# Performance work log

Hardware: AMD Instinct MI355X
Metric: run time of the kernel (lower is better)

## Reference

```python
import jax, jax.numpy as jnp
import numpy as np

B, S, D, H, FF = 4, 1024, 1024, 16, 4096
HD = D // H
EPS = 1e-5


def _layernorm(x, g, b):
    m = x.mean(-1, keepdims=True)
    v = ((x - m) ** 2).mean(-1, keepdims=True)
    return g * (x - m) / jnp.sqrt(v + EPS) + b


def _heads(t):  # [B,S,D] -> [B,H,S,HD]
    return t.reshape(t.shape[0], t.shape[1], H, HD).transpose(0, 2, 1, 3)


def _attn(q, k, v):  # manual scaled-dot-product, returns [B,S,D]
    s = jnp.einsum('bhqd,bhkd->bhqk', q, k) / jnp.sqrt(jnp.float32(HD))
    a = jax.nn.softmax(s, axis=-1)
    o = jnp.einsum('bhqk,bhkd->bhqd', a, v)
    return o.transpose(0, 2, 1, 3).reshape(q.shape[0], q.shape[2], D)


def _proj(x, w, b):  # torch linear: x @ w.T + b
    return x @ w.T + b


def setup_inputs() -> dict:
    key = jax.random.key(0)
    ks = jax.random.split(key, 32)
    i = iter(range(32))
    act = lambda sh: jax.random.normal(ks[next(i)], sh, dtype=jnp.float32)
    wgt = lambda sh: jax.random.normal(ks[next(i)], sh, dtype=jnp.float32) * 0.02
    inp = {
        'x': act((B, S, D)), 'y': act((B, S, D)),
        'decoder_mask': jnp.zeros((1,), jnp.float32),
        'image_outputs': act((B, S, D)), 'constant_y': act((B, S, D)),
        'image_query_weight': wgt((D, D)), 'image_query_bias': wgt((D,)),
        'image_key_weight': wgt((D, D)), 'image_key_bias': wgt((D,)),
        'image_value_weight': wgt((D, D)), 'image_value_bias': wgt((D,)),
        'audio_query_weight': wgt((D, D)), 'audio_query_bias': wgt((D,)),
        'audio_key_weight': wgt((D, D)), 'audio_key_bias': wgt((D,)),
        'audio_value_weight': wgt((D, D)), 'audio_value_bias': wgt((D,)),
        'self_out_w': wgt((D, D)), 'self_out_b': wgt((D,)),
        'cross_out_w': wgt((D, D)), 'cross_out_b': wgt((D,)),
        'ffn_w1': wgt((FF, D)), 'ffn_b1': wgt((FF,)),
        'ffn_w2': wgt((D, FF)), 'ffn_b2': wgt((D,)),
        'gamma1': jnp.ones((D,), jnp.float32), 'beta1': jnp.zeros((D,), jnp.float32),
        'gamma2': jnp.ones((D,), jnp.float32), 'beta2': jnp.zeros((D,), jnp.float32),
        'gamma3': jnp.ones((D,), jnp.float32), 'beta3': jnp.zeros((D,), jnp.float32),
    }
    return inp


def reference(x, y, decoder_mask, image_outputs, constant_y,
              image_query_weight, image_query_bias, image_key_weight, image_key_bias,
              image_value_weight, image_value_bias,
              audio_query_weight, audio_query_bias, audio_key_weight, audio_key_bias,
              audio_value_weight, audio_value_bias,
              self_out_w, self_out_b, cross_out_w, cross_out_b,
              ffn_w1, ffn_b1, ffn_w2, ffn_b2,
              gamma1, beta1, gamma2, beta2, gamma3, beta3):
    # count == 0 path; mask is overwritten to None in the original; eval mode (no dropout)
    # --- self-attention: Q,K,V all from image_outputs with image weights ---
    q = _heads(_proj(image_outputs, image_query_weight, image_query_bias))
    k = _heads(_proj(image_outputs, image_key_weight, image_key_bias))
    v = _heads(_proj(image_outputs, image_value_weight, image_value_bias))
    sa = _proj(_attn(q, k, v), self_out_w, self_out_b)
    sa = jax.lax.stop_gradient(sa)  # out.detach().clone()
    y1 = _layernorm(sa + y, gamma1, beta1)
    # --- cross-attention: Q from constant_y (image query weights), K,V from x (audio weights) ---
    q = _heads(_proj(constant_y, image_query_weight, image_query_bias))
    k = _heads(_proj(x, audio_key_weight, audio_key_bias))
    v = _heads(_proj(x, audio_value_weight, audio_value_bias))
    ca = _proj(_attn(q, k, v), cross_out_w, cross_out_b)
    ca = jax.lax.stop_gradient(ca)
    y2 = _layernorm(ca + y1, gamma2, beta2)
    # --- FFN (hidden detached after relu in original) ---
    h = jax.lax.stop_gradient(jax.nn.relu(_proj(y2, ffn_w1, ffn_b1)))
    ff = _proj(h, ffn_w2, ffn_b2)
    y3 = _layernorm(ff + y2, gamma3, beta3)
    return y3
```

## Files before the change

kernel.cpp:

```cpp
#include <hip/hip_runtime.h>

typedef unsigned short u16;
typedef __attribute__((ext_vector_type(8))) short bf16x8;
typedef __attribute__((ext_vector_type(8))) unsigned short u16x8;
typedef __attribute__((ext_vector_type(4))) float f32x4;

__device__ __forceinline__ float bf2f(u16 x) {
  return __uint_as_float(((unsigned)x) << 16);
}
__device__ __forceinline__ u16 f2bf(float f) {
  unsigned u = __float_as_uint(f);
  unsigned r = (u + 0x7FFFu + ((u >> 16) & 1u)) >> 16;
  return (u16)r;
}

#define GLD_LDS16(g, l)                                                        \
  __builtin_amdgcn_global_load_lds(                                            \
      (const __attribute__((address_space(1))) void*)(g),                      \
      (__attribute__((address_space(3))) void*)(l), 16, 0, 0)
#define MFMA16(a, b, c) __builtin_amdgcn_mfma_f32_16x16x32_bf16(a, b, c, 0, 0, 0)

struct CvtSegs {
  const float* src[12];
  u16* dst[12];
  int cum[13];
};

__global__ __launch_bounds__(256) void cvt_all(CvtSegs p) {
  int blk = blockIdx.x, s = 0;
  while (blk >= p.cum[s + 1]) ++s;
  size_t off = (size_t)(blk - p.cum[s]) * 1024 + threadIdx.x * 4;
  float4 v = *(const float4*)(p.src[s] + off);
  ushort4 o;
  o.x = f2bf(v.x); o.y = f2bf(v.y); o.z = f2bf(v.z); o.w = f2bf(v.w);
  *(ushort4*)(p.dst[s] + off) = o;
}

struct GemmMulti {
  const u16* A[3]; const u16* W[3]; u16* C[3];
  const float* bias[3][4];
  u16* VT[3];
  int v_start[3];
  int N[3];
  int xbase[4];
  int K, relu;
};

template <int BM, int BN>
__global__ __launch_bounds__(256, 2) void gemm_k(GemmMulti g) {
  constexpr int MI = BM / 32, NI = BN / 32;
  constexpr int CA = BM / 32, CB = BN / 32;
  __shared__ __align__(16) u16 As[BM * 64];
  __shared__ __align__(16) u16 Bs[BN * 64];
  const int bx = blockIdx.x;
  int ri = 0;
  if (bx >= g.xbase[1]) ri = (bx >= g.xbase[2]) ? 2 : 1;
  const u16* __restrict__ A = g.A[ri];
  const u16* __restrict__ W = g.W[ri];
  u16* __restrict__ C = g.C[ri];
  const int K = g.K, N = g.N[ri];
  const int tid = threadIdx.x, lane = tid & 63, w = tid >> 6;
  const int l16 = lane & 15, quad = lane >> 4;
  const int wr = w >> 1, wc = w & 1;
  const int m0 = blockIdx.y * BM, n0 = (bx - g.xbase[ri]) * BN;

  f32x4 acc[MI][NI];
#pragma unroll
  for (int i = 0; i < MI; ++i)
#pragma unroll
    for (int j = 0; j < NI; ++j) acc[i][j] = (f32x4){0.f, 0.f, 0.f, 0.f};

  size_t offA[CA]; int ldsA[CA];
#pragma unroll
  for (int t = 0; t < CA; ++t) {
    int idx = w * CA + t;
    int r = idx * 8 + (lane >> 3);
    int gs = (lane & 7) ^ (r & 7);
    offA[t] = (size_t)(m0 + r) * K + gs * 8;
    ldsA[t] = idx * 512;
  }
  size_t offB[CB]; int ldsB[CB];
#pragma unroll
  for (int t = 0; t < CB; ++t) {
    int idx = w * CB + t;
    int r = idx * 8 + (lane >> 3);
    int gs = (lane & 7) ^ (r & 7);
    offB[t] = (size_t)(n0 + r) * K + gs * 8;
    ldsB[t] = idx * 512;
  }

  for (int k0 = 0; k0 < K; k0 += 64) {
    __syncthreads();
#pragma unroll
    for (int t = 0; t < CA; ++t) GLD_LDS16(A + offA[t] + k0, &As[ldsA[t]]);
#pragma unroll
    for (int t = 0; t < CB; ++t) GLD_LDS16(W + offB[t] + k0, &Bs[ldsB[t]]);
    __syncthreads();
#pragma unroll
    for (int ks = 0; ks < 2; ++ks) {
      const int gk = ks * 4 + quad;
      bf16x8 af[MI], bfr[NI];
#pragma unroll
      for (int mi = 0; mi < MI; ++mi) {
        int m = wr * (BM / 2) + mi * 16 + l16;
        af[mi] = *(const bf16x8*)&As[m * 64 + ((gk ^ (m & 7)) * 8)];
      }
#pragma unroll
      for (int ni = 0; ni < NI; ++ni) {
        int n = wc * (BN / 2) + ni * 16 + l16;
        bfr[ni] = *(const bf16x8*)&Bs[n * 64 + ((gk ^ (n & 7)) * 8)];
      }
#pragma unroll
      for (int mi = 0; mi < MI; ++mi)
#pragma unroll
        for (int ni = 0; ni < NI; ++ni)
          acc[mi][ni] = MFMA16(af[mi], bfr[ni], acc[mi][ni]);
    }
  }

  u16* VT = g.VT[ri];
  const int vs = g.v_start[ri];
#pragma unroll
  for (int ni = 0; ni < NI; ++ni) {
    int n = n0 + wc * (BN / 2) + ni * 16 + l16;
    float bv = g.bias[ri][n >> 10][n & 1023];
    bool inV = (VT != nullptr) && (n >= vs);
#pragma unroll
    for (int mi = 0; mi < MI; ++mi) {
      int mr = m0 + wr * (BM / 2) + mi * 16 + quad * 4;
      float v0 = acc[mi][ni][0] + bv, v1 = acc[mi][ni][1] + bv;
      float v2 = acc[mi][ni][2] + bv, v3 = acc[mi][ni][3] + bv;
      if (g.relu) {
        v0 = fmaxf(v0, 0.f); v1 = fmaxf(v1, 0.f);
        v2 = fmaxf(v2, 0.f); v3 = fmaxf(v3, 0.f);
      }
      if (inV) {
        int d = n - vs;
        size_t base = ((size_t)((mr >> 10) * 16 + (d >> 6)) * 64 + (d & 63)) * 1024;
        ushort4 pk;
        pk.x = f2bf(v0); pk.y = f2bf(v1); pk.z = f2bf(v2); pk.w = f2bf(v3);
        *(ushort4*)(VT + base + (mr & 1023)) = pk;
      } else {
        C[(size_t)(mr + 0) * N + n] = f2bf(v0);
        C[(size_t)(mr + 1) * N + n] = f2bf(v1);
        C[(size_t)(mr + 2) * N + n] = f2bf(v2);
        C[(size_t)(mr + 3) * N + n] = f2bf(v3);
      }
    }
  }
}

struct AttnArgs {
  const u16* Q[2]; const u16* K[2]; const u16* VT[2]; u16* O[2];
  int ldq[2], ldk[2];
};

__global__ __launch_bounds__(256, 2) void attn_fwd(AttnArgs p) {
  __shared__ __align__(16) float Red[4][64 * 68];
  __shared__ __align__(16) float Lred[4][68];
  const int bid = blockIdx.x;
  const int sbh = bid & 127, qt = bid >> 7;
  const int set = sbh >> 6, b = (sbh >> 4) & 3, h = sbh & 15;
  const int tid = threadIdx.x, lane = tid & 63, w = tid >> 6;
  const int l16 = lane & 15, quad = lane >> 4;
  const int l7 = l16 & 7, lc = l16 >> 3;

  const u16* __restrict__ Qg = p.Q[set];
  const u16* __restrict__ Kg = p.K[set];
  const u16* __restrict__ Vg = p.VT[set];
  u16* __restrict__ Og = p.O[set];
  const int ldq = p.ldq[set], ldk = p.ldk[set];
  const size_t qoff = (size_t)b * 1024 * ldq + h * 64;
  const size_t koff = (size_t)b * 1024 * ldk + h * 64;
  const size_t voff = (size_t)(b * 16 + h) * 64 * 1024;
  const size_t ooff = (size_t)b * 1024 * 1024 + h * 64;

  bf16x8 aq[4][2];
#pragma unroll
  for (int mi = 0; mi < 4; ++mi)
#pragma unroll
    for (int hh = 0; hh < 2; ++hh)
      aq[mi][hh] = *(const bf16x8*)(Qg + qoff +
          (size_t)(qt * 64 + mi * 16 + l16) * ldq + hh * 32 + quad * 8);

  const short s1 = 0x3F80;
  const bf16x8 ones = {s1, s1, s1, s1, s1, s1, s1, s1};

  f32x4 o[4][4], lacc[4];
#pragma unroll
  for (int mi = 0; mi < 4; ++mi) {
    lacc[mi] = (f32x4){0.f, 0.f, 0.f, 0.f};
#pragma unroll
    for (int dg = 0; dg < 4; ++dg) o[mi][dg] = (f32x4){0.f, 0.f, 0.f, 0.f};
  }

  u16* Ps = (u16*)&Red[w][0];

  for (int t = 0; t < 4; ++t) {
    const int k0 = (w * 4 + t) * 64;
    bf16x8 bk[4][2], bv[4][2];
#pragma unroll
    for (int nn = 0; nn < 4; ++nn)
#pragma unroll
      for (int hh = 0; hh < 2; ++hh) {
        bk[nn][hh] = *(const bf16x8*)(Kg + koff +
            (size_t)(k0 + nn * 16 + l16) * ldk + hh * 32 + quad * 8);
        bv[nn][hh] = *(const bf16x8*)(Vg + voff +
            (size_t)(nn * 16 + l16) * 1024 + k0 + hh * 32 + quad * 8);
      }
#pragma unroll
    for (int mi = 0; mi < 4; ++mi) {
      f32x4 sc[4];
#pragma unroll
      for (int nn = 0; nn < 4; ++nn) {
        f32x4 z = (f32x4){0.f, 0.f, 0.f, 0.f};
        z = MFMA16(aq[mi][0], bk[nn][0], z);
        z = MFMA16(aq[mi][1], bk[nn][1], z);
        sc[nn] = z;
      }
#pragma unroll
      for (int nn = 0; nn < 4; ++nn) {
        const int cc = nn * 2 + lc;
#pragma unroll
        for (int r = 0; r < 4; ++r) {
          const int m = quad * 4 + r;
          float pv = __expf(fmaf(sc[nn][r], 0.125f, -30.0f));
          Ps[mi * 1024 + m * 64 + ((cc ^ (m & 7)) * 8) + l7] =
              (u16)(__float_as_uint(pv) >> 16);
        }
      }
      bf16x8 ap0 = *(const bf16x8*)&Ps[mi * 1024 + l16 * 64 + ((quad ^ l7) * 8)];
      bf16x8 ap1 = *(const bf16x8*)&Ps[mi * 1024 + l16 * 64 + (((4 + quad) ^ l7) * 8)];
#pragma unroll
      for (int dg = 0; dg < 4; ++dg) {
        o[mi][dg] = MFMA16(ap0, bv[dg][0], o[mi][dg]);
        o[mi][dg] = MFMA16(ap1, bv[dg][1], o[mi][dg]);
      }
      lacc[mi] = MFMA16(ap0, ones, lacc[mi]);
      lacc[mi] = MFMA16(ap1, ones, lacc[mi]);
    }
  }

#pragma unroll
  for (int dg = 0; dg < 4; ++dg)
#pragma unroll
    for (int mi = 0; mi < 4; ++mi)
      *(f32x4*)&Red[w][(dg * 16 + l16) * 68 + mi * 16 + quad * 4] = o[mi][dg];
  if (l16 == 0) {
#pragma unroll
    for (int mi = 0; mi < 4; ++mi)
      *(f32x4*)&Lred[w][mi * 16 + quad * 4] = lacc[mi];
  }
  __syncthreads();

  f32x4 lt = (f32x4){0.f, 0.f, 0.f, 0.f};
#pragma unroll
  for (int j = 0; j < 4; ++j) lt += *(const f32x4*)&Lred[j][w * 16 + quad * 4];
  f32x4 inv;
#pragma unroll
  for (int r = 0; r < 4; ++r) inv[r] = 1.f / lt[r];
#pragma unroll
  for (int dg = 0; dg < 4; ++dg) {
    f32x4 os = (f32x4){0.f, 0.f, 0.f, 0.f};
#pragma unroll
    for (int j = 0; j < 4; ++j)
      os += *(const f32x4*)&Red[j][(dg * 16 + l16) * 68 + w * 16 + quad * 4];
#pragma unroll
    for (int r = 0; r < 4; ++r)
      Og[ooff + (size_t)(qt * 64 + w * 16 + quad * 4 + r) * 1024 + dg * 16 + l16] =
          f2bf(os[r] * inv[r]);
  }
}

template <int BF32, int OF32>
__global__ __launch_bounds__(256) void ln_add(
    const u16* __restrict__ A, const u16* __restrict__ Bb,
    const float* __restrict__ Bf,
    const float* __restrict__ G, const float* __restrict__ Bt,
    u16* __restrict__ Ob, float* __restrict__ Of)
{
  __shared__ float red[8];
  const int row = blockIdx.x, t = threadIdx.x;
  const int w = t >> 6, lane = t & 63;
  size_t off = (size_t)row * 1024 + t * 4;
  union { ushort4 v; u16 e[4]; } av;
  av.v = *(const ushort4*)(A + off);
  float x[4], s = 0.f, s2 = 0.f;
  if (BF32) {
    float4 bv = *(const float4*)(Bf + off);
    x[0] = bf2f(av.e[0]) + bv.x; x[1] = bf2f(av.e[1]) + bv.y;
    x[2] = bf2f(av.e[2]) + bv.z; x[3] = bf2f(av.e[3]) + bv.w;
  } else {
    union { ushort4 v; u16 e[4]; } bv;
    bv.v = *(const ushort4*)(Bb + off);
#pragma unroll
    for (int i = 0; i < 4; ++i) x[i] = bf2f(av.e[i]) + bf2f(bv.e[i]);
  }
#pragma unroll
  for (int i = 0; i < 4; ++i) { s += x[i]; s2 += x[i] * x[i]; }
#pragma unroll
  for (int d = 32; d >= 1; d >>= 1) {
    s += __shfl_xor(s, d);
    s2 += __shfl_xor(s2, d);
  }
  if (lane == 0) { red[w] = s; red[4 + w] = s2; }
  __syncthreads();
  s = red[0] + red[1] + red[2] + red[3];
  s2 = red[4] + red[5] + red[6] + red[7];
  float mean = s * (1.f / 1024.f);
  float var = s2 * (1.f / 1024.f) - mean * mean;
  float rstd = rsqrtf(var + 1e-5f);
  float4 gv = *(const float4*)(G + t * 4);
  float4 bev = *(const float4*)(Bt + t * 4);
  float yv[4];
  yv[0] = (x[0] - mean) * rstd * gv.x + bev.x;
  yv[1] = (x[1] - mean) * rstd * gv.y + bev.y;
  yv[2] = (x[2] - mean) * rstd * gv.z + bev.z;
  yv[3] = (x[3] - mean) * rstd * gv.w + bev.w;
  if (OF32) {
    float4 ov = {yv[0], yv[1], yv[2], yv[3]};
    *(float4*)(Of + off) = ov;
  } else {
    ushort4 ov;
    ov.x = f2bf(yv[0]); ov.y = f2bf(yv[1]); ov.z = f2bf(yv[2]); ov.w = f2bf(yv[3]);
    *(ushort4*)(Ob + off) = ov;
  }
}

extern "C" void kernel_launch(void* const* d_in, const int* in_sizes, int n_in,
                              void* d_out, int out_size, void* d_ws, size_t ws_size,
                              hipStream_t stream)
{
  (void)in_sizes; (void)n_in; (void)out_size; (void)ws_size;
  const float* x   = (const float*)d_in[0];
  const float* y   = (const float*)d_in[1];
  const float* img = (const float*)d_in[3];
  const float* cy  = (const float*)d_in[4];
  const float* iqw = (const float*)d_in[5];  const float* iqb = (const float*)d_in[6];
  const float* ikw = (const float*)d_in[7];  const float* ikb = (const float*)d_in[8];
  const float* ivw = (const float*)d_in[9];  const float* ivb = (const float*)d_in[10];
  const float* akw = (const float*)d_in[13]; const float* akb = (const float*)d_in[14];
  const float* avw = (const float*)d_in[15]; const float* avb = (const float*)d_in[16];
  const float* sow = (const float*)d_in[17]; const float* sob = (const float*)d_in[18];
  const float* cow = (const float*)d_in[19]; const float* cob = (const float*)d_in[20];
  const float* w1  = (const float*)d_in[21]; const float* b1  = (const float*)d_in[22];
  const float* w2  = (const float*)d_in[23]; const float* b2  = (const float*)d_in[24];
  const float* g1  = (const float*)d_in[25]; const float* be1 = (const float*)d_in[26];
  const float* g2  = (const float*)d_in[27]; const float* be2 = (const float*)d_in[28];
  const float* g3  = (const float*)d_in[29]; const float* be3 = (const float*)d_in[30];

  u16* ws = (u16*)d_ws;
  const size_t T = (size_t)4 * 1024 * 1024;
  const size_t M1 = (size_t)1024 * 1024;
  u16* img_b = ws + 0 * T;               u16* bao_s = ws + 0 * T;  u16* bff = ws + 0 * T;
  u16* cy_b  = ws + 1 * T;               u16* bao_c = ws + 1 * T;
  u16* x_b   = ws + 2 * T;               u16* bp_s  = ws + 2 * T;
  u16* bqkv  = ws + 3 * T;       u16* bp_c  = ws + 3 * T;
                                         u16* by1   = ws + 4 * T;
                                         u16* by2   = ws + 5 * T;
  u16* vt_s  = ws + 6 * T;
  u16* vt_c  = ws + 7 * T;               u16* bh    = ws + 7 * T;
  u16* bq_c  = ws + 8 * T;
  u16* bkv_c = ws + 9 * T;
  u16* wb    = ws + 11 * T;
  u16* sow_b = wb + 5 * M1;  u16* cow_b = wb + 6 * M1;
  u16* w1_b  = wb + 7 * M1;  u16* w2_b  = wb + 11 * M1;

  dim3 blk(256);

  CvtSegs cv;
  const float* srcs[12] = {img, cy, x, iqw, ikw, ivw, akw, avw, sow, cow, w1, w2};
  u16* dsts[12] = {img_b, cy_b, x_b, wb, wb + M1, wb + 2 * M1, wb + 3 * M1,
                   wb + 4 * M1, sow_b, cow_b, w1_b, w2_b};
  int nblk[12] = {4096, 4096, 4096, 1024, 1024, 1024, 1024, 1024, 1024, 1024,
                  4096, 4096};
  int c = 0;
  for (int i = 0; i < 12; ++i) { cv.src[i] = srcs[i]; cv.dst[i] = dsts[i]; }
  cv.cum[0] = 0;
  for (int i = 0; i < 12; ++i) { c += nblk[i]; cv.cum[i + 1] = c; }
  cvt_all<<<c, blk, 0, stream>>>(cv);

  {
    GemmMulti g{};
    g.A[0] = img_b; g.W[0] = wb;          g.C[0] = bqkv;  g.N[0] = 3072;
    g.VT[0] = vt_s; g.v_start[0] = 2048;
    g.bias[0][0] = iqb; g.bias[0][1] = ikb; g.bias[0][2] = ivb; g.bias[0][3] = ivb;
    g.A[1] = cy_b;  g.W[1] = wb;          g.C[1] = bq_c;  g.N[1] = 1024;
    g.VT[1] = nullptr; g.v_start[1] = 0;
    g.bias[1][0] = iqb; g.bias[1][1] = iqb; g.bias[1][2] = iqb; g.bias[1][3] = iqb;
    g.A[2] = x_b;   g.W[2] = wb + 3 * M1; g.C[2] = bkv_c; g.N[2] = 2048;
    g.VT[2] = vt_c; g.v_start[2] = 1024;
    g.bias[2][0] = akb; g.bias[2][1] = avb; g.bias[2][2] = avb; g.bias[2][3] = avb;
    g.xbase[0] = 0; g.xbase[1] = 24; g.xbase[2] = 32; g.xbase[3] = 48;
    g.K = 1024; g.relu = 0;
    gemm_k<128, 128><<<dim3(48, 32), blk, 0, stream>>>(g);
  }

  {
    AttnArgs a{};
    a.Q[0] = bqkv; a.K[0] = bqkv + 1024; a.VT[0] = vt_s; a.O[0] = bao_s;
    a.ldq[0] = 3072; a.ldk[0] = 3072;
    a.Q[1] = bq_c; a.K[1] = bkv_c;       a.VT[1] = vt_c; a.O[1] = bao_c;
    a.ldq[1] = 1024; a.ldk[1] = 2048;
    attn_fwd<<<2048, blk, 0, stream>>>(a);
  }

  {
    GemmMulti g{};
    g.A[0] = bao_s; g.W[0] = sow_b; g.C[0] = bp_s; g.N[0] = 1024;
    g.bias[0][0] = sob; g.bias[0][1] = sob; g.bias[0][2] = sob; g.bias[0][3] = sob;
    g.A[1] = bao_c; g.W[1] = cow_b; g.C[1] = bp_c; g.N[1] = 1024;
    g.bias[1][0] = cob; g.bias[1][1] = cob; g.bias[1][2] = cob; g.bias[1][3] = cob;
    g.A[2] = bao_s; g.W[2] = sow_b; g.C[2] = bp_s; g.N[2] = 1024;
    g.bias[2][0] = sob; g.bias[2][1] = sob; g.bias[2][2] = sob; g.bias[2][3] = sob;
    g.xbase[0] = 0; g.xbase[1] = 8; g.xbase[2] = 16; g.xbase[3] = 16;
    g.K = 1024; g.relu = 0;
    gemm_k<128, 128><<<dim3(16, 32), blk, 0, stream>>>(g);
  }

  ln_add<1, 0><<<4096, blk, 0, stream>>>(bp_s, nullptr, y, g1, be1, by1, nullptr);
  ln_add<0, 0><<<4096, blk, 0, stream>>>(bp_c, by1, nullptr, g2, be2, by2, nullptr);

  {
    GemmMulti g{};
    g.A[0] = by2; g.W[0] = w1_b; g.C[0] = bh; g.N[0] = 4096;
    g.bias[0][0] = b1; g.bias[0][1] = b1 + 1024; g.bias[0][2] = b1 + 2048;
    g.bias[0][3] = b1 + 3072;
    g.A[1] = by2; g.W[1] = w1_b; g.C[1] = bh; g.N[1] = 4096;
    g.bias[1][0] = b1; g.bias[1][1] = b1; g.bias[1][2] = b1; g.bias[1][3] = b1;
    g.A[2] = g.A[1]; g.W[2] = g.W[1]; g.C[2] = g.C[1]; g.N[2] = 4096;
    g.bias[2][0] = b1; g.bias[2][1] = b1; g.bias[2][2] = b1; g.bias[2][3] = b1;
    g.xbase[0] = 0; g.xbase[1] = 32; g.xbase[2] = 32; g.xbase[3] = 32;
    g.K = 1024; g.relu = 1;
    gemm_k<128, 128><<<dim3(32, 32), blk, 0, stream>>>(g);
  }
  {
    GemmMulti g{};
    g.A[0] = bh; g.W[0] = w2_b; g.C[0] = bff; g.N[0] = 1024;
    g.bias[0][0] = b2; g.bias[0][1] = b2; g.bias[0][2] = b2; g.bias[0][3] = b2;
    g.A[1] = bh; g.W[1] = w2_b; g.C[1] = bff; g.N[1] = 1024;
    g.bias[1][0] = b2; g.bias[1][1] = b2; g.bias[1][2] = b2; g.bias[1][3] = b2;
    g.A[2] = g.A[1]; g.W[2] = g.W[1]; g.C[2] = g.C[1]; g.N[2] = 1024;
    g.bias[2][0] = b2; g.bias[2][1] = b2; g.bias[2][2] = b2; g.bias[2][3] = b2;
    g.xbase[0] = 0; g.xbase[1] = 16; g.xbase[2] = 16; g.xbase[3] = 16;
    g.K = 4096; g.relu = 0;
    gemm_k<128, 64><<<dim3(16, 32), blk, 0, stream>>>(g);
  }

  ln_add<0, 1><<<4096, blk, 0, stream>>>(bff, by2, nullptr, g3, be3, nullptr,
                                         (float*)d_out);
}
```

Measured before the change: 499.2 us.

## Halve attention LDS footprint with two-stage reduction and raise occupancy hints

The attention kernel now reuses a single 1024-element P tile per wave instead of one per mi, and shrinks the cross-wave reduction buffer from four slices to two. Waves 2-3 deposit their partial O and row sums, waves 0-1 fold them in, then all waves sum the two slices. This cuts LDS per block so more blocks fit per CU, and launch bounds for both gemm and attention go from 2 to 3 waves-per-EU. The exp is rewritten as exp2 with prescaled constants. In exchange there are extra barriers and LDS round trips in the epilogue, and the tighter register cap may cause spills in the GEMM.

```diff
diff --git a/kernel.cpp b/kernel.cpp
--- a/kernel.cpp
+++ b/kernel.cpp
@@ -47,7 +47,7 @@
 };
 
 template <int BM, int BN>
-__global__ __launch_bounds__(256, 2) void gemm_k(GemmMulti g) {
+__global__ __launch_bounds__(256, 3) void gemm_k(GemmMulti g) {
   constexpr int MI = BM / 32, NI = BN / 32;
   constexpr int CA = BM / 32, CB = BN / 32;
   __shared__ __align__(16) u16 As[BM * 64];
@@ -155,9 +155,9 @@
   int ldq[2], ldk[2];
 };
 
-__global__ __launch_bounds__(256, 2) void attn_fwd(AttnArgs p) {
-  __shared__ __align__(16) float Red[4][64 * 68];
-  __shared__ __align__(16) float Lred[4][68];
+__global__ __launch_bounds__(256, 3) void attn_fwd(AttnArgs p) {
+  __shared__ __align__(16) float Red[2][64 * 68];
+  __shared__ __align__(16) float Lred[2][64];
   const int bid = blockIdx.x;
   const int sbh = bid & 127, qt = bid >> 7;
   const int set = sbh >> 6, b = (sbh >> 4) & 3, h = sbh & 15;
@@ -194,7 +194,7 @@
     for (int dg = 0; dg < 4; ++dg) o[mi][dg] = (f32x4){0.f, 0.f, 0.f, 0.f};
   }
 
-  u16* Ps = (u16*)&Red[w][0];
+  u16* Ps = (u16*)(&Red[0][0]) + w * 1024;
 
   for (int t = 0; t < 4; ++t) {
     const int k0 = (w * 4 + t) * 64;
@@ -224,13 +224,13 @@
 #pragma unroll
         for (int r = 0; r < 4; ++r) {
           const int m = quad * 4 + r;
-          float pv = __expf(fmaf(sc[nn][r], 0.125f, -30.0f));
-          Ps[mi * 1024 + m * 64 + ((cc ^ (m & 7)) * 8) + l7] =
+          float pv = exp2f(fmaf(sc[nn][r], 0.1803368801f, -43.2808512f));
+          Ps[m * 64 + ((cc ^ (m & 7)) * 8) + l7] =
               (u16)(__float_as_uint(pv) >> 16);
         }
       }
-      bf16x8 ap0 = *(const bf16x8*)&Ps[mi * 1024 + l16 * 64 + ((quad ^ l7) * 8)];
-      bf16x8 ap1 = *(const bf16x8*)&Ps[mi * 1024 + l16 * 64 + (((4 + quad) ^ l7) * 8)];
+      bf16x8 ap0 = *(const bf16x8*)&Ps[l16 * 64 + ((quad ^ l7) * 8)];
+      bf16x8 ap1 = *(const bf16x8*)&Ps[l16 * 64 + (((4 + quad) ^ l7) * 8)];
 #pragma unroll
       for (int dg = 0; dg < 4; ++dg) {
         o[mi][dg] = MFMA16(ap0, bv[dg][0], o[mi][dg]);
@@ -241,30 +241,58 @@
     }
   }
 
-#pragma unroll
-  for (int dg = 0; dg < 4; ++dg)
-#pragma unroll
-    for (int mi = 0; mi < 4; ++mi)
-      *(f32x4*)&Red[w][(dg * 16 + l16) * 68 + mi * 16 + quad * 4] = o[mi][dg];
-  if (l16 == 0) {
-#pragma unroll
-    for (int mi = 0; mi < 4; ++mi)
-      *(f32x4*)&Lred[w][mi * 16 + quad * 4] = lacc[mi];
-  }
   __syncthreads();
-
-  f32x4 lt = (f32x4){0.f, 0.f, 0.f, 0.f};
-#pragma unroll
-  for (int j = 0; j < 4; ++j) lt += *(const f32x4*)&Lred[j][w * 16 + quad * 4];
-  f32x4 inv;
+  if (w >= 2) {
+    float* buf = Red[w - 2];
+#pragma unroll
+    for (int dg = 0; dg < 4; ++dg)
+#pragma unroll
+      for (int mi = 0; mi < 4; ++mi)
+        *(f32x4*)&buf[(dg * 16 + l16) * 68 + mi * 16 + quad * 4] = o[mi][dg];
+    if (l16 == 0) {
+#pragma unroll
+      for (int mi = 0; mi < 4; ++mi)
+        *(f32x4*)&Lred[w - 2][mi * 16 + quad * 4] = lacc[mi];
+    }
+  }
+  __syncthreads();
+  if (w < 2) {
+    float* buf = Red[w];
+#pragma unroll
+    for (int dg = 0; dg < 4; ++dg)
+#pragma unroll
+      for (int mi = 0; mi < 4; ++mi) {
+        f32x4 pv = *(const f32x4*)&buf[(dg * 16 + l16) * 68 + mi * 16 + quad * 4];
+        o[mi][dg] += pv;
+      }
+#pragma unroll
+    for (int mi = 0; mi < 4; ++mi) {
+      f32x4 lv = *(const f32x4*)&Lred[w][mi * 16 + quad * 4];
+      lacc[mi] += lv;
+    }
+#pragma unroll
+    for (int dg = 0; dg < 4; ++dg)
+#pragma unroll
+      for (int mi = 0; mi < 4; ++mi)
+        *(f32x4*)&buf[(dg * 16 + l16) * 68 + mi * 16 + quad * 4] = o[mi][dg];
+    if (l16 == 0) {
+#pragma unroll
+      for (int mi = 0; mi < 4; ++mi)
+        *(f32x4*)&Lred[w][mi * 16 + quad * 4] = lacc[mi];
+    }
+  }
+  __syncthreads();
+
+  f32x4 l0 = *(const f32x4*)&Lred[0][w * 16 + quad * 4];
+  f32x4 l1 = *(const f32x4*)&Lred[1][w * 16 + quad * 4];
+  f32x4 lt = l0 + l1, inv;
 #pragma unroll
   for (int r = 0; r < 4; ++r) inv[r] = 1.f / lt[r];
 #pragma unroll
   for (int dg = 0; dg < 4; ++dg) {
-    f32x4 os = (f32x4){0.f, 0.f, 0.f, 0.f};
-#pragma unroll
-    for (int j = 0; j < 4; ++j)
-      os += *(const f32x4*)&Red[j][(dg * 16 + l16) * 68 + w * 16 + quad * 4];
+    f32x4 a0 = *(const f32x4*)&Red[0][(dg * 16 + l16) * 68 + w * 16 + quad * 4];
+    f32x4 a1 = *(const f32x4*)&Red[1][(dg * 16 + l16) * 68 + w * 16 + quad * 4];
+    f32x4 os = a0 + a1;
 #pragma unroll
     for (int r = 0; r < 4; ++r)
       Og[ooff + (size_t)(qt * 64 + w * 16 + quad * 4 + r) * 1024 + dg * 16 + l16] =
```

Result: slower. 632.2 us (+26.6%).
